# Optimization experiments

Hardware: AMD Instinct MI355X
Metric: run time of the kernel (lower is better)

## Reference

```python
import jax, jax.numpy as jnp
import numpy as np

D_MODEL = 256
N_HEAD = 4
HEAD_DIM = D_MODEL // N_HEAD  # 64


def setup_inputs() -> dict:
    key = jax.random.key(0)
    kx, kw, kb = jax.random.split(key, 3)
    x = jax.random.normal(kx, (4, 2048, D_MODEL), dtype=jnp.float32)
    # nn.Linear(256, 768): weight [768, 256], bias [768]
    bound = 1.0 / np.sqrt(D_MODEL)
    W_qkv = jax.random.uniform(kw, (3 * D_MODEL, D_MODEL), dtype=jnp.float32, minval=-bound, maxval=bound)
    b_qkv = jax.random.uniform(kb, (3 * D_MODEL,), dtype=jnp.float32, minval=-bound, maxval=bound)
    return {"x": x, "W_qkv": W_qkv, "b_qkv": b_qkv}


def reference(x, W_qkv, b_qkv):
    B, S, _ = x.shape
    # fused QKV projection: [B, S, 3*D]
    qkv = jnp.einsum("bsd,ed->bse", x, W_qkv) + b_qkv
    q, k, v = jnp.split(qkv, 3, axis=-1)
    # [B, S, D] -> [B, H, S, Dh]
    def to_heads(t):
        return t.reshape(B, S, N_HEAD, HEAD_DIM).transpose(0, 2, 1, 3)
    q, k, v = to_heads(q), to_heads(k), to_heads(v)
    scale = 1.0 / np.sqrt(HEAD_DIM)
    # scores [B, H, S, S]
    scores = jnp.einsum("bhqd,bhkd->bhqk", q, k) * scale
    attn = jax.nn.softmax(scores, axis=-1)
    out = jnp.einsum("bhqk,bhkd->bhqd", attn, v)  # [B, H, S, Dh]
    return out
```

## Files before the change

### kernel.cpp

```cpp
#include <hip/hip_runtime.h>

#define BB 4
#define SS 2048
#define DM 256
#define NH 4
#define DH 64
#define NROW (BB*SS)
#define NE   (3*DM)
#define BH   (BB*NH)
#define HEAD_ELEMS (BH*SS*DH)
#define NQROWS (BH*SS)

typedef _Float16 half_t;
typedef __attribute__((ext_vector_type(8))) _Float16 half8;
typedef __attribute__((ext_vector_type(4))) _Float16 half4;
typedef __attribute__((ext_vector_type(4))) float floatx4;

#define KPAD 72

__global__ __launch_bounds__(256) void prep(const float* __restrict__ x,
                                            const float* __restrict__ W,
                                            half_t* __restrict__ xh,
                                            half_t* __restrict__ xl,
                                            half_t* __restrict__ wh) {
    int gtid = blockIdx.x * 256 + threadIdx.x;
    {
        int i = gtid * 4;
        float4 v = *(const float4*)&x[i];
        half4 h, l;
        h.x = (half_t)v.x; l.x = (half_t)(v.x - (float)h.x);
        h.y = (half_t)v.y; l.y = (half_t)(v.y - (float)h.y);
        h.z = (half_t)v.z; l.z = (half_t)(v.z - (float)h.z);
        h.w = (half_t)v.w; l.w = (half_t)(v.w - (float)h.w);
        *(half4*)&xh[i] = h;
        *(half4*)&xl[i] = l;
    }
    if (gtid < NE * DM / 4) {
        int i = gtid * 4;
        float4 v = *(const float4*)&W[i];
        half4 h;
        h.x = (half_t)v.x; h.y = (half_t)v.y;
        h.z = (half_t)v.z; h.w = (half_t)v.w;
        *(half4*)&wh[i] = h;
    }
}

__global__ __launch_bounds__(256) void qkv_proj(const half_t* __restrict__ xh,
                                                const half_t* __restrict__ xl,
                                                const half_t* __restrict__ whg,
                                                const float* __restrict__ bias,
                                                half_t* __restrict__ qh,
                                                half_t* __restrict__ kh,
                                                half_t* __restrict__ vt) {
    __shared__ __align__(16) half_t Xh[64 * KPAD];
    __shared__ __align__(16) half_t Xl[64 * KPAD];
    __shared__ __align__(16) half_t Wh[64 * KPAD];

    const int rb   = blockIdx.x * 64;
    const int nb   = blockIdx.y * 64;
    const int tid  = threadIdx.x;
    const int wid  = tid >> 6;
    const int lane = tid & 63;
    const int quad = lane >> 4;
    const int col  = lane & 15;

    floatx4 acc[4];
    #pragma unroll
    for (int t = 0; t < 4; ++t) acc[t] = (floatx4){0.f, 0.f, 0.f, 0.f};

    for (int k0 = 0; k0 < DM; k0 += 64) {
        __syncthreads();
        #pragma unroll
        for (int i = 0; i < 2; ++i) {
            int gi = tid + 256 * i;
            int r  = gi >> 3;
            int c8 = (gi & 7) * 8;
            *(half8*)&Xh[r * KPAD + c8] = *(const half8*)&xh[(size_t)(rb + r) * DM + k0 + c8];
            *(half8*)&Xl[r * KPAD + c8] = *(const half8*)&xl[(size_t)(rb + r) * DM + k0 + c8];
            *(half8*)&Wh[r * KPAD + c8] = *(const half8*)&whg[(size_t)(nb + r) * DM + k0 + c8];
        }
        __syncthreads();

        half8 ah0 = *(const half8*)&Xh[(wid * 16 + col) * KPAD + quad * 8];
        half8 ah1 = *(const half8*)&Xh[(wid * 16 + col) * KPAD + 32 + quad * 8];
        half8 al0 = *(const half8*)&Xl[(wid * 16 + col) * KPAD + quad * 8];
        half8 al1 = *(const half8*)&Xl[(wid * 16 + col) * KPAD + 32 + quad * 8];

        #pragma unroll
        for (int t = 0; t < 4; ++t) {
            half8 bh0 = *(const half8*)&Wh[(t * 16 + col) * KPAD + quad * 8];
            half8 bh1 = *(const half8*)&Wh[(t * 16 + col) * KPAD + 32 + quad * 8];
            acc[t] = __builtin_amdgcn_mfma_f32_16x16x32_f16(ah0, bh0, acc[t], 0, 0, 0);
            acc[t] = __builtin_amdgcn_mfma_f32_16x16x32_f16(ah1, bh1, acc[t], 0, 0, 0);
            acc[t] = __builtin_amdgcn_mfma_f32_16x16x32_f16(al0, bh0, acc[t], 0, 0, 0);
            acc[t] = __builtin_amdgcn_mfma_f32_16x16x32_f16(al1, bh1, acc[t], 0, 0, 0);
        }
    }

    const int part = nb >> 8;
    const int mloc = wid * 16 + quad * 4;
    if (part != 2) {
        #pragma unroll
        for (int t = 0; t < 4; ++t) {
            int e    = nb + t * 16 + col;
            float be = bias[e];
            int dm   = e & 255;
            int h    = dm >> 6;
            int dh   = dm & 63;
            #pragma unroll
            for (int r = 0; r < 4; ++r) {
                int row = rb + mloc + r;
                int b   = row >> 11;
                int s   = row & 2047;
                int bh_ = b * NH + h;
                float val = acc[t][r] + be;
                if (part == 0) {
                    qh[((size_t)bh_ * SS + s) * DH + dh] = (half_t)(val * 0.125f);
                } else {
                    kh[((size_t)bh_ * SS + s) * DH + dh] = (half_t)val;
                }
            }
        }
    } else {
        __syncthreads();
        #pragma unroll
        for (int t = 0; t < 4; ++t) {
            int e    = nb + t * 16 + col;
            float be = bias[e];
            #pragma unroll
            for (int r = 0; r < 4; ++r)
                Xh[(t * 16 + col) * KPAD + mloc + r] = (half_t)(acc[t][r] + be);
        }
        __syncthreads();
        const int b   = rb >> 11;
        const int s0  = rb & 2047;
        const int h   = (nb >> 6) & 3;
        const int bh_ = b * NH + h;
        #pragma unroll
        for (int i = 0; i < 2; ++i) {
            int idx = tid + 256 * i;
            int rr  = idx >> 3;
            int cc8 = (idx & 7) * 8;
            *(half8*)&vt[((size_t)bh_ * DH + rr) * SS + s0 + cc8] =
                *(const half8*)&Xh[rr * KPAD + cc8];
        }
    }
}

__global__ __launch_bounds__(128) void attn(const half_t* __restrict__ qh,
                                            const half_t* __restrict__ kh,
                                            const half_t* __restrict__ vt,
                                            half_t* __restrict__ pO,
                                            float* __restrict__ mst,
                                            float* __restrict__ lst) {
    __shared__ __align__(16) half_t Ks[64 * KPAD];
    __shared__ __align__(16) half_t Vts[64 * KPAD];

    const int q0   = blockIdx.x * 64;
    const int bh   = blockIdx.y;
    const int kz   = blockIdx.z;
    const size_t base = (size_t)bh * SS * DH;
    const int tid  = threadIdx.x;
    const int wid  = tid >> 6;
    const int lane = tid & 63;
    const int quad = lane >> 4;
    const int col  = lane & 15;
    const int ktBeg = kz * (SS / 2);
    const int ktEnd = ktBeg + (SS / 2);

    int srr[4], scc[4];
    #pragma unroll
    for (int i = 0; i < 4; ++i) {
        int gi = tid + 128 * i;
        srr[i] = gi >> 3;
        scc[i] = (gi & 7) * 8;
    }

    half8 bq[2][2];
    #pragma unroll
    for (int st = 0; st < 2; ++st) {
        int s = q0 + wid * 32 + st * 16 + col;
        bq[st][0] = *(const half8*)&qh[base + (size_t)s * DH + quad * 8];
        bq[st][1] = *(const half8*)&qh[base + (size_t)s * DH + 32 + quad * 8];
    }

    half8 ck[4], cv[4], nk[4], nv[4];
    #pragma unroll
    for (int i = 0; i < 4; ++i) {
        ck[i] = *(const half8*)&kh[base + (size_t)(ktBeg + srr[i]) * DH + scc[i]];
        cv[i] = *(const half8*)&vt[base + (size_t)srr[i] * SS + ktBeg + scc[i]];
        nk[i] = ck[i];
        nv[i] = cv[i];
    }

    float m_i[2] = {-3.0e38f, -3.0e38f};
    float l_i[2] = {0.f, 0.f};
    floatx4 o[2][4];
    #pragma unroll
    for (int st = 0; st < 2; ++st)
        #pragma unroll
        for (int dt = 0; dt < 4; ++dt) o[st][dt] = (floatx4){0.f, 0.f, 0.f, 0.f};

    for (int kt = ktBeg; kt < ktEnd; kt += 64) {
        __syncthreads();
        #pragma unroll
        for (int i = 0; i < 4; ++i) {
            *(half8*)&Ks[srr[i] * KPAD + scc[i]]  = ck[i];
            *(half8*)&Vts[srr[i] * KPAD + scc[i]] = cv[i];
        }
        __syncthreads();

        const int ktn = kt + 64;
        if (ktn < ktEnd) {
            #pragma unroll
            for (int i = 0; i < 4; ++i) {
                nk[i] = *(const half8*)&kh[base + (size_t)(ktn + srr[i]) * DH + scc[i]];
                nv[i] = *(const half8*)&vt[base + (size_t)srr[i] * SS + ktn + scc[i]];
            }
        }

        floatx4 sc[2][4];
        #pragma unroll
        for (int t = 0; t < 4; ++t) {
            half8 ak0 = *(const half8*)&Ks[(t * 16 + col) * KPAD + quad * 8];
            half8 ak1 = *(const half8*)&Ks[(t * 16 + col) * KPAD + 32 + quad * 8];
            #pragma unroll
            for (int st = 0; st < 2; ++st) {
                floatx4 c = (floatx4){0.f, 0.f, 0.f, 0.f};
                c = __builtin_amdgcn_mfma_f32_16x16x32_f16(ak0, bq[st][0], c, 0, 0, 0);
                c = __builtin_amdgcn_mfma_f32_16x16x32_f16(ak1, bq[st][1], c, 0, 0, 0);
                sc[st][t] = c;
            }
        }

        half4 pa[2][4];
        #pragma unroll
        for (int st = 0; st < 2; ++st) {
            float mloc = -3.0e38f;
            #pragma unroll
            for (int t = 0; t < 4; ++t)
                #pragma unroll
                for (int r = 0; r < 4; ++r)
                    mloc = fmaxf(mloc, sc[st][t][r]);
            mloc = fmaxf(mloc, __shfl_xor(mloc, 16));
            mloc = fmaxf(mloc, __shfl_xor(mloc, 32));
            float m_new = fmaxf(m_i[st], mloc);
            float alpha = __expf(m_i[st] - m_new);
            m_i[st] = m_new;

            float rsum = 0.f;
            #pragma unroll
            for (int t = 0; t < 4; ++t) {
                float p0 = __expf(sc[st][t][0] - m_new);
                float p1 = __expf(sc[st][t][1] - m_new);
                float p2 = __expf(sc[st][t][2] - m_new);
                float p3 = __expf(sc[st][t][3] - m_new);
                rsum += p0 + p1 + p2 + p3;
                pa[st][t] = (half4){(half_t)p0, (half_t)p1, (half_t)p2, (half_t)p3};
            }
            rsum += __shfl_xor(rsum, 16);
            rsum += __shfl_xor(rsum, 32);
            l_i[st] = l_i[st] * alpha + rsum;

            float ar[4];
            #pragma unroll
            for (int i = 0; i < 4; ++i) ar[i] = __shfl(alpha, quad * 4 + i);
            #pragma unroll
            for (int dt = 0; dt < 4; ++dt)
                #pragma unroll
                for (int i = 0; i < 4; ++i)
                    o[st][dt][i] *= ar[i];
        }

        #pragma unroll
        for (int t = 0; t < 4; ++t) {
            #pragma unroll
            for (int dt = 0; dt < 4; ++dt) {
                half4 bv = *(const half4*)&Vts[(dt * 16 + col) * KPAD + t * 16 + quad * 4];
                #pragma unroll
                for (int st = 0; st < 2; ++st)
                    o[st][dt] = __builtin_amdgcn_mfma_f32_16x16x16f16(pa[st][t], bv, o[st][dt], 0, 0, 0);
            }
        }

        #pragma unroll
        for (int i = 0; i < 4; ++i) { ck[i] = nk[i]; cv[i] = nv[i]; }
    }

    const size_t pbase = (size_t)kz * HEAD_ELEMS + base;
    #pragma unroll
    for (int st = 0; st < 2; ++st) {
        float inv = 1.0f / l_i[st];
        float ir[4];
        #pragma unroll
        for (int i = 0; i < 4; ++i) ir[i] = __shfl(inv, quad * 4 + i);
        #pragma unroll
        for (int dt = 0; dt < 4; ++dt)
            #pragma unroll
            for (int i = 0; i < 4; ++i) {
                int row = q0 + wid * 32 + st * 16 + quad * 4 + i;
                pO[pbase + (size_t)row * DH + dt * 16 + col] = (half_t)(o[st][dt][i] * ir[i]);
            }
        if (quad == 0) {
            int row = q0 + wid * 32 + st * 16 + col;
            int idx = kz * NQROWS + bh * SS + row;
            mst[idx] = m_i[st];
            lst[idx] = l_i[st];
        }
    }
}

__global__ __launch_bounds__(256) void merge(const half_t* __restrict__ pO,
                                             const float* __restrict__ mst,
                                             const float* __restrict__ lst,
                                             float* __restrict__ out) {
    int gid = blockIdx.x * 256 + threadIdx.x;
    int row = gid >> 3;
    int dc  = (gid & 7) * 8;
    float m1 = mst[row], m2 = mst[NQROWS + row];
    float l1 = lst[row], l2 = lst[NQROWS + row];
    float M  = fmaxf(m1, m2);
    float w1 = l1 * __expf(m1 - M);
    float w2 = l2 * __expf(m2 - M);
    float inv = 1.0f / (w1 + w2);
    float a = w1 * inv, b = w2 * inv;
    half8 o1 = *(const half8*)&pO[(size_t)row * DH + dc];
    half8 o2 = *(const half8*)&pO[(size_t)HEAD_ELEMS + (size_t)row * DH + dc];
    float4 r0, r1;
    r0.x = a * (float)o1[0] + b * (float)o2[0];
    r0.y = a * (float)o1[1] + b * (float)o2[1];
    r0.z = a * (float)o1[2] + b * (float)o2[2];
    r0.w = a * (float)o1[3] + b * (float)o2[3];
    r1.x = a * (float)o1[4] + b * (float)o2[4];
    r1.y = a * (float)o1[5] + b * (float)o2[5];
    r1.z = a * (float)o1[6] + b * (float)o2[6];
    r1.w = a * (float)o1[7] + b * (float)o2[7];
    *(float4*)&out[(size_t)row * DH + dc]     = r0;
    *(float4*)&out[(size_t)row * DH + dc + 4] = r1;
}

extern "C" void kernel_launch(void* const* d_in, const int* in_sizes, int n_in,
                              void* d_out, int out_size, void* d_ws, size_t ws_size,
                              hipStream_t stream) {
    const float* x  = (const float*)d_in[0];
    const float* Wq = (const float*)d_in[1];
    const float* bq = (const float*)d_in[2];
    float* out = (float*)d_out;

    half_t* qh  = (half_t*)d_ws;
    half_t* kh  = qh + (size_t)HEAD_ELEMS;
    half_t* vt  = kh + (size_t)HEAD_ELEMS;
    half_t* xh  = vt + (size_t)HEAD_ELEMS;
    half_t* xl  = xh + (size_t)HEAD_ELEMS;
    half_t* whp = xl + (size_t)HEAD_ELEMS;
    half_t* pO  = xh;
    float*  mst = (float*)((char*)d_ws + 21364736);
    float*  lst = mst + 2 * NQROWS;

    prep<<<2048, 256, 0, stream>>>(x, Wq, xh, xl, whp);
    qkv_proj<<<dim3(NROW / 64, NE / 64), 256, 0, stream>>>(xh, xl, whp, bq, qh, kh, vt);
    attn<<<dim3(SS / 64, BH, 2), 128, 0, stream>>>(qh, kh, vt, pO, mst, lst);
    merge<<<1024, 256, 0, stream>>>(pO, mst, lst, out);
}
```

Baseline: 120.6 us.

## Drop LDS staging in projection and attention; load MFMA fragments from global directly

The QKV projection now has each wave load its MFMA operands straight from global memory. Each block covers 128 rows instead of 64, and shared memory is used only for the V transpose. The attention kernel likewise drops its shared-memory K/V tiles and barriers, reading K and V fragments into registers with K prefetched one tile ahead. It also skips the softmax rescale when no row max grows. Together these remove LDS traffic and __syncthreads stalls, at the cost of more uncoalesced global and cache loads and higher register pressure.

```diff
diff --git a/kernel.cpp b/kernel.cpp
--- a/kernel.cpp
+++ b/kernel.cpp
@@ -16,7 +16,7 @@
 typedef __attribute__((ext_vector_type(4))) _Float16 half4;
 typedef __attribute__((ext_vector_type(4))) float floatx4;
 
-#define KPAD 72
+#define VPAD 136
 
 __global__ __launch_bounds__(256) void prep(const float* __restrict__ x,
                                             const float* __restrict__ W,
@@ -52,110 +52,102 @@
                                                 half_t* __restrict__ qh,
                                                 half_t* __restrict__ kh,
                                                 half_t* __restrict__ vt) {
-    __shared__ __align__(16) half_t Xh[64 * KPAD];
-    __shared__ __align__(16) half_t Xl[64 * KPAD];
-    __shared__ __align__(16) half_t Wh[64 * KPAD];
-
-    const int rb   = blockIdx.x * 64;
+    __shared__ __align__(16) half_t Vtile[64 * VPAD];
+
     const int nb   = blockIdx.y * 64;
     const int tid  = threadIdx.x;
     const int wid  = tid >> 6;
     const int lane = tid & 63;
     const int quad = lane >> 4;
     const int col  = lane & 15;
-
-    floatx4 acc[4];
-    #pragma unroll
-    for (int t = 0; t < 4; ++t) acc[t] = (floatx4){0.f, 0.f, 0.f, 0.f};
-
-    for (int k0 = 0; k0 < DM; k0 += 64) {
+    const int rb   = blockIdx.x * 128 + wid * 32;
+
+    floatx4 acc[2][4];
+    #pragma unroll
+    for (int st = 0; st < 2; ++st)
+        #pragma unroll
+        for (int t = 0; t < 4; ++t) acc[st][t] = (floatx4){0.f, 0.f, 0.f, 0.f};
+
+    #pragma unroll
+    for (int k0 = 0; k0 < DM; k0 += 32) {
+        half8 ah[2], al[2], bw[4];
+        #pragma unroll
+        for (int st = 0; st < 2; ++st) {
+            const size_t ro = (size_t)(rb + st * 16 + col) * DM + k0 + quad * 8;
+            ah[st] = *(const half8*)&xh[ro];
+            al[st] = *(const half8*)&xl[ro];
+        }
+        #pragma unroll
+        for (int t = 0; t < 4; ++t)
+            bw[t] = *(const half8*)&whg[(size_t)(nb + t * 16 + col) * DM + k0 + quad * 8];
+        #pragma unroll
+        for (int t = 0; t < 4; ++t)
+            #pragma unroll
+            for (int st = 0; st < 2; ++st) {
+                acc[st][t] = __builtin_amdgcn_mfma_f32_16x16x32_f16(ah[st], bw[t], acc[st][t], 0, 0, 0);
+                acc[st][t] = __builtin_amdgcn_mfma_f32_16x16x32_f16(al[st], bw[t], acc[st][t], 0, 0, 0);
+            }
+    }
+
+    const int part = nb >> 8;
+    if (part != 2) {
+        #pragma unroll
+        for (int st = 0; st < 2; ++st)
+            #pragma unroll
+            for (int t = 0; t < 4; ++t) {
+                int e    = nb + t * 16 + col;
+                float be = bias[e];
+                int dm   = e & 255;
+                int h    = dm >> 6;
+                int dh   = dm & 63;
+                #pragma unroll
+                for (int r = 0; r < 4; ++r) {
+                    int row = rb + st * 16 + quad * 4 + r;
+                    int b   = row >> 11;
+                    int s   = row & 2047;
+                    int bh_ = b * NH + h;
+                    float val = acc[st][t][r] + be;
+                    if (part == 0) {
+                        qh[((size_t)bh_ * SS + s) * DH + dh] = (half_t)(val * 0.125f);
+                    } else {
+                        kh[((size_t)bh_ * SS + s) * DH + dh] = (half_t)val;
+                    }
+                }
+            }
+    } else {
+        #pragma unroll
+        for (int st = 0; st < 2; ++st)
+            #pragma unroll
+            for (int t = 0; t < 4; ++t) {
+                int e    = nb + t * 16 + col;
+                float be = bias[e];
+                #pragma unroll
+                for (int r = 0; r < 4; ++r)
+                    Vtile[(t * 16 + col) * VPAD + wid * 32 + st * 16 + quad * 4 + r] =
+                        (half_t)(acc[st][t][r] + be);
+            }
         __syncthreads();
-        #pragma unroll
-        for (int i = 0; i < 2; ++i) {
-            int gi = tid + 256 * i;
-            int r  = gi >> 3;
-            int c8 = (gi & 7) * 8;
-            *(half8*)&Xh[r * KPAD + c8] = *(const half8*)&xh[(size_t)(rb + r) * DM + k0 + c8];
-            *(half8*)&Xl[r * KPAD + c8] = *(const half8*)&xl[(size_t)(rb + r) * DM + k0 + c8];
-            *(half8*)&Wh[r * KPAD + c8] = *(const half8*)&whg[(size_t)(nb + r) * DM + k0 + c8];
-        }
-        __syncthreads();
-
-        half8 ah0 = *(const half8*)&Xh[(wid * 16 + col) * KPAD + quad * 8];
-        half8 ah1 = *(const half8*)&Xh[(wid * 16 + col) * KPAD + 32 + quad * 8];
-        half8 al0 = *(const half8*)&Xl[(wid * 16 + col) * KPAD + quad * 8];
-        half8 al1 = *(const half8*)&Xl[(wid * 16 + col) * KPAD + 32 + quad * 8];
-
-        #pragma unroll
-        for (int t = 0; t < 4; ++t) {
-            half8 bh0 = *(const half8*)&Wh[(t * 16 + col) * KPAD + quad * 8];
-            half8 bh1 = *(const half8*)&Wh[(t * 16 + col) * KPAD + 32 + quad * 8];
-            acc[t] = __builtin_amdgcn_mfma_f32_16x16x32_f16(ah0, bh0, acc[t], 0, 0, 0);
-            acc[t] = __builtin_amdgcn_mfma_f32_16x16x32_f16(ah1, bh1, acc[t], 0, 0, 0);
-            acc[t] = __builtin_amdgcn_mfma_f32_16x16x32_f16(al0, bh0, acc[t], 0, 0, 0);
-            acc[t] = __builtin_amdgcn_mfma_f32_16x16x32_f16(al1, bh1, acc[t], 0, 0, 0);
-        }
-    }
-
-    const int part = nb >> 8;
-    const int mloc = wid * 16 + quad * 4;
-    if (part != 2) {
-        #pragma unroll
-        for (int t = 0; t < 4; ++t) {
-            int e    = nb + t * 16 + col;
-            float be = bias[e];
-            int dm   = e & 255;
-            int h    = dm >> 6;
-            int dh   = dm & 63;
-            #pragma unroll
-            for (int r = 0; r < 4; ++r) {
-                int row = rb + mloc + r;
-                int b   = row >> 11;
-                int s   = row & 2047;
-                int bh_ = b * NH + h;
-                float val = acc[t][r] + be;
-                if (part == 0) {
-                    qh[((size_t)bh_ * SS + s) * DH + dh] = (half_t)(val * 0.125f);
-                } else {
-                    kh[((size_t)bh_ * SS + s) * DH + dh] = (half_t)val;
-                }
-            }
-        }
-    } else {
-        __syncthreads();
-        #pragma unroll
-        for (int t = 0; t < 4; ++t) {
-            int e    = nb + t * 16 + col;
-            float be = bias[e];
-            #pragma unroll
-            for (int r = 0; r < 4; ++r)
-                Xh[(t * 16 + col) * KPAD + mloc + r] = (half_t)(acc[t][r] + be);
-        }
-        __syncthreads();
-        const int b   = rb >> 11;
-        const int s0  = rb & 2047;
+        const int s0  = (blockIdx.x * 128) & 2047;
+        const int b   = (blockIdx.x * 128) >> 11;
         const int h   = (nb >> 6) & 3;
         const int bh_ = b * NH + h;
         #pragma unroll
-        for (int i = 0; i < 2; ++i) {
-            int idx = tid + 256 * i;
-            int rr  = idx >> 3;
-            int cc8 = (idx & 7) * 8;
-            *(half8*)&vt[((size_t)bh_ * DH + rr) * SS + s0 + cc8] =
-                *(const half8*)&Xh[rr * KPAD + cc8];
-        }
-    }
-}
-
-__global__ __launch_bounds__(128) void attn(const half_t* __restrict__ qh,
-                                            const half_t* __restrict__ kh,
-                                            const half_t* __restrict__ vt,
-                                            half_t* __restrict__ pO,
-                                            float* __restrict__ mst,
-                                            float* __restrict__ lst) {
-    __shared__ __align__(16) half_t Ks[64 * KPAD];
-    __shared__ __align__(16) half_t Vts[64 * KPAD];
-
+        for (int i = 0; i < 4; ++i) {
+            int gi = tid + 256 * i;
+            int rr = gi >> 4;
+            int cc = (gi & 15) * 8;
+            *(half8*)&vt[((size_t)bh_ * DH + rr) * SS + s0 + cc] =
+                *(const half8*)&Vtile[rr * VPAD + cc];
+        }
+    }
+}
+
+__global__ __launch_bounds__(128, 2) void attn(const half_t* __restrict__ qh,
+                                               const half_t* __restrict__ kh,
+                                               const half_t* __restrict__ vt,
+                                               half_t* __restrict__ pO,
+                                               float* __restrict__ mst,
+                                               float* __restrict__ lst) {
     const int q0   = blockIdx.x * 64;
     const int bh   = blockIdx.y;
     const int kz   = blockIdx.z;
@@ -168,14 +160,6 @@
     const int ktBeg = kz * (SS / 2);
     const int ktEnd = ktBeg + (SS / 2);
 
-    int srr[4], scc[4];
-    #pragma unroll
-    for (int i = 0; i < 4; ++i) {
-        int gi = tid + 128 * i;
-        srr[i] = gi >> 3;
-        scc[i] = (gi & 7) * 8;
-    }
-
     half8 bq[2][2];
     #pragma unroll
     for (int st = 0; st < 2; ++st) {
@@ -184,13 +168,12 @@
         bq[st][1] = *(const half8*)&qh[base + (size_t)s * DH + 32 + quad * 8];
     }
 
-    half8 ck[4], cv[4], nk[4], nv[4];
-    #pragma unroll
-    for (int i = 0; i < 4; ++i) {
-        ck[i] = *(const half8*)&kh[base + (size_t)(ktBeg + srr[i]) * DH + scc[i]];
-        cv[i] = *(const half8*)&vt[base + (size_t)srr[i] * SS + ktBeg + scc[i]];
-        nk[i] = ck[i];
-        nv[i] = cv[i];
+    half8 ck[2][4];
+    #pragma unroll
+    for (int t = 0; t < 4; ++t) {
+        const size_t kro = base + (size_t)(ktBeg + t * 16 + col) * DH + quad * 8;
+        ck[0][t] = *(const half8*)&kh[kro];
+        ck[1][t] = *(const half8*)&kh[kro + 32];
     }
 
     float m_i[2] = {-3.0e38f, -3.0e38f};
@@ -202,35 +185,32 @@
         for (int dt = 0; dt < 4; ++dt) o[st][dt] = (floatx4){0.f, 0.f, 0.f, 0.f};
 
     for (int kt = ktBeg; kt < ktEnd; kt += 64) {
-        __syncthreads();
-        #pragma unroll
-        for (int i = 0; i < 4; ++i) {
-            *(half8*)&Ks[srr[i] * KPAD + scc[i]]  = ck[i];
-            *(half8*)&Vts[srr[i] * KPAD + scc[i]] = cv[i];
-        }
-        __syncthreads();
-
-        const int ktn = kt + 64;
-        if (ktn < ktEnd) {
-            #pragma unroll
-            for (int i = 0; i < 4; ++i) {
-                nk[i] = *(const half8*)&kh[base + (size_t)(ktn + srr[i]) * DH + scc[i]];
-                nv[i] = *(const half8*)&vt[base + (size_t)srr[i] * SS + ktn + scc[i]];
-            }
-        }
+        half4 cv[4][4];
+        #pragma unroll
+        for (int t = 0; t < 4; ++t)
+            #pragma unroll
+            for (int dt = 0; dt < 4; ++dt)
+                cv[t][dt] = *(const half4*)&vt[base + (size_t)(dt * 16 + col) * SS +
+                                               kt + t * 16 + quad * 4];
 
         floatx4 sc[2][4];
         #pragma unroll
-        for (int t = 0; t < 4; ++t) {
-            half8 ak0 = *(const half8*)&Ks[(t * 16 + col) * KPAD + quad * 8];
-            half8 ak1 = *(const half8*)&Ks[(t * 16 + col) * KPAD + 32 + quad * 8];
+        for (int t = 0; t < 4; ++t)
             #pragma unroll
             for (int st = 0; st < 2; ++st) {
                 floatx4 c = (floatx4){0.f, 0.f, 0.f, 0.f};
-                c = __builtin_amdgcn_mfma_f32_16x16x32_f16(ak0, bq[st][0], c, 0, 0, 0);
-                c = __builtin_amdgcn_mfma_f32_16x16x32_f16(ak1, bq[st][1], c, 0, 0, 0);
+                c = __builtin_amdgcn_mfma_f32_16x16x32_f16(ck[0][t], bq[st][0], c, 0, 0, 0);
+                c = __builtin_amdgcn_mfma_f32_16x16x32_f16(ck[1][t], bq[st][1], c, 0, 0, 0);
                 sc[st][t] = c;
             }
+
+        const int ktn = (kt + 64 < ktEnd) ? kt + 64 : ktBeg;
+        half8 nk[2][4];
+        #pragma unroll
+        for (int t = 0; t < 4; ++t) {
+            const size_t kro = base + (size_t)(ktn + t * 16 + col) * DH + quad * 8;
+            nk[0][t] = *(const half8*)&kh[kro];
+            nk[1][t] = *(const half8*)&kh[kro + 32];
         }
 
         half4 pa[2][4];
@@ -244,10 +224,23 @@
                     mloc = fmaxf(mloc, sc[st][t][r]);
             mloc = fmaxf(mloc, __shfl_xor(mloc, 16));
             mloc = fmaxf(mloc, __shfl_xor(mloc, 32));
-            float m_new = fmaxf(m_i[st], mloc);
-            float alpha = __expf(m_i[st] - m_new);
-            m_i[st] = m_new;
-
+
+            if (__any(mloc > m_i[st])) {
+                float m_new = fmaxf(m_i[st], mloc);
+                float alpha = __expf(m_i[st] - m_new);
+                m_i[st] = m_new;
+                l_i[st] *= alpha;
+                float ar[4];
+                #pragma unroll
+                for (int i = 0; i < 4; ++i) ar[i] = __shfl(alpha, quad * 4 + i);
+                #pragma unroll
+                for (int dt = 0; dt < 4; ++dt)
+                    #pragma unroll
+                    for (int i = 0; i < 4; ++i)
+                        o[st][dt][i] *= ar[i];
+            }
+
+            float m_new = m_i[st];
             float rsum = 0.f;
             #pragma unroll
             for (int t = 0; t < 4; ++t) {
@@ -260,31 +253,21 @@
             }
             rsum += __shfl_xor(rsum, 16);
             rsum += __shfl_xor(rsum, 32);
-            l_i[st] = l_i[st] * alpha + rsum;
-
-            float ar[4];
-            #pragma unroll
-            for (int i = 0; i < 4; ++i) ar[i] = __shfl(alpha, quad * 4 + i);
-            #pragma unroll
-            for (int dt = 0; dt < 4; ++dt)
-                #pragma unroll
-                for (int i = 0; i < 4; ++i)
-                    o[st][dt][i] *= ar[i];
-        }
-
-        #pragma unroll
-        for (int t = 0; t < 4; ++t) {
+            l_i[st] += rsum;
+        }
+
+        #pragma unroll
+        for (int t = 0; t < 4; ++t)
             #pragma unroll
             for (int dt = 0; dt < 4; ++dt) {
-                half4 bv = *(const half4*)&Vts[(dt * 16 + col) * KPAD + t * 16 + quad * 4];
+                half4 bv = cv[t][dt];
                 #pragma unroll
                 for (int st = 0; st < 2; ++st)
                     o[st][dt] = __builtin_amdgcn_mfma_f32_16x16x16f16(pa[st][t], bv, o[st][dt], 0, 0, 0);
             }
-        }
-
-        #pragma unroll
-        for (int i = 0; i < 4; ++i) { ck[i] = nk[i]; cv[i] = nv[i]; }
+
+        #pragma unroll
+        for (int t = 0; t < 4; ++t) { ck[0][t] = nk[0][t]; ck[1][t] = nk[1][t]; }
     }
 
     const size_t pbase = (size_t)kz * HEAD_ELEMS + base;
@@ -358,7 +341,7 @@
     float*  lst = mst + 2 * NQROWS;
 
     prep<<<2048, 256, 0, stream>>>(x, Wq, xh, xl, whp);
-    qkv_proj<<<dim3(NROW / 64, NE / 64), 256, 0, stream>>>(xh, xl, whp, bq, qh, kh, vt);
+    qkv_proj<<<dim3(NROW / 128, NE / 64), 256, 0, stream>>>(xh, xl, whp, bq, qh, kh, vt);
     attn<<<dim3(SS / 64, BH, 2), 128, 0, stream>>>(qh, kh, vt, pO, mst, lst);
     merge<<<1024, 256, 0, stream>>>(pO, mst, lst, out);
 }
```

New measurement: 183.4 us. 1.52x slower.

## Split attention into up to four KV chunks and restructure QKV projection loads

Applied to the files above, without the earlier changes.

The QKV projection now stages the full 64x256 X tile (high and low halves) in LDS once and reads W fragments straight from global memory, removing the per-k-step barriers. The softmax switches to exp2 with log2(e) folded into the Q scale. The attention kernel drops the separate prefetch registers and gains an occupancy hint. When the workspace is large enough it splits the KV range four ways instead of two, with a generalized merge. The aim is more parallelism and less barrier and register overhead, at the cost of extra partial-output traffic and a merge that now runs runtime-length loops.

```diff
diff --git a/kernel.cpp b/kernel.cpp
--- a/kernel.cpp
+++ b/kernel.cpp
@@ -17,6 +17,8 @@
 typedef __attribute__((ext_vector_type(4))) float floatx4;
 
 #define KPAD 72
+#define XPAD 264
+#define QSCALE 0.1803368801111120f
 
 __global__ __launch_bounds__(256) void prep(const float* __restrict__ x,
                                             const float* __restrict__ W,
@@ -52,9 +54,8 @@
                                                 half_t* __restrict__ qh,
                                                 half_t* __restrict__ kh,
                                                 half_t* __restrict__ vt) {
-    __shared__ __align__(16) half_t Xh[64 * KPAD];
-    __shared__ __align__(16) half_t Xl[64 * KPAD];
-    __shared__ __align__(16) half_t Wh[64 * KPAD];
+    __shared__ __align__(16) half_t Xh2[64 * XPAD];
+    __shared__ __align__(16) half_t Xl2[64 * XPAD];
 
     const int rb   = blockIdx.x * 64;
     const int nb   = blockIdx.y * 64;
@@ -64,36 +65,33 @@
     const int quad = lane >> 4;
     const int col  = lane & 15;
 
+    #pragma unroll
+    for (int i = 0; i < 8; ++i) {
+        int gi = tid + 256 * i;
+        int r  = gi >> 5;
+        int c8 = (gi & 31) * 8;
+        *(half8*)&Xh2[r * XPAD + c8] = *(const half8*)&xh[(size_t)(rb + r) * DM + c8];
+        *(half8*)&Xl2[r * XPAD + c8] = *(const half8*)&xl[(size_t)(rb + r) * DM + c8];
+    }
+    __syncthreads();
+
     floatx4 acc[4];
     #pragma unroll
     for (int t = 0; t < 4; ++t) acc[t] = (floatx4){0.f, 0.f, 0.f, 0.f};
 
-    for (int k0 = 0; k0 < DM; k0 += 64) {
-        __syncthreads();
-        #pragma unroll
-        for (int i = 0; i < 2; ++i) {
-            int gi = tid + 256 * i;
-            int r  = gi >> 3;
-            int c8 = (gi & 7) * 8;
-            *(half8*)&Xh[r * KPAD + c8] = *(const half8*)&xh[(size_t)(rb + r) * DM + k0 + c8];
-            *(half8*)&Xl[r * KPAD + c8] = *(const half8*)&xl[(size_t)(rb + r) * DM + k0 + c8];
-            *(half8*)&Wh[r * KPAD + c8] = *(const half8*)&whg[(size_t)(nb + r) * DM + k0 + c8];
-        }
-        __syncthreads();
-
-        half8 ah0 = *(const half8*)&Xh[(wid * 16 + col) * KPAD + quad * 8];
-        half8 ah1 = *(const half8*)&Xh[(wid * 16 + col) * KPAD + 32 + quad * 8];
-        half8 al0 = *(const half8*)&Xl[(wid * 16 + col) * KPAD + quad * 8];
-        half8 al1 = *(const half8*)&Xl[(wid * 16 + col) * KPAD + 32 + quad * 8];
-
-        #pragma unroll
-        for (int t = 0; t < 4; ++t) {
-            half8 bh0 = *(const half8*)&Wh[(t * 16 + col) * KPAD + quad * 8];
-            half8 bh1 = *(const half8*)&Wh[(t * 16 + col) * KPAD + 32 + quad * 8];
-            acc[t] = __builtin_amdgcn_mfma_f32_16x16x32_f16(ah0, bh0, acc[t], 0, 0, 0);
-            acc[t] = __builtin_amdgcn_mfma_f32_16x16x32_f16(ah1, bh1, acc[t], 0, 0, 0);
-            acc[t] = __builtin_amdgcn_mfma_f32_16x16x32_f16(al0, bh0, acc[t], 0, 0, 0);
-            acc[t] = __builtin_amdgcn_mfma_f32_16x16x32_f16(al1, bh1, acc[t], 0, 0, 0);
+    const int arow = (wid * 16 + col) * XPAD + quad * 8;
+    #pragma unroll
+    for (int k0 = 0; k0 < DM; k0 += 32) {
+        half8 bw[4];
+        #pragma unroll
+        for (int t = 0; t < 4; ++t)
+            bw[t] = *(const half8*)&whg[(size_t)(nb + t * 16 + col) * DM + k0 + quad * 8];
+        half8 ah = *(const half8*)&Xh2[arow + k0];
+        half8 al = *(const half8*)&Xl2[arow + k0];
+        #pragma unroll
+        for (int t = 0; t < 4; ++t) {
+            acc[t] = __builtin_amdgcn_mfma_f32_16x16x32_f16(ah, bw[t], acc[t], 0, 0, 0);
+            acc[t] = __builtin_amdgcn_mfma_f32_16x16x32_f16(al, bw[t], acc[t], 0, 0, 0);
         }
     }
 
@@ -115,7 +113,7 @@
                 int bh_ = b * NH + h;
                 float val = acc[t][r] + be;
                 if (part == 0) {
-                    qh[((size_t)bh_ * SS + s) * DH + dh] = (half_t)(val * 0.125f);
+                    qh[((size_t)bh_ * SS + s) * DH + dh] = (half_t)(val * QSCALE);
                 } else {
                     kh[((size_t)bh_ * SS + s) * DH + dh] = (half_t)val;
                 }
@@ -129,7 +127,7 @@
             float be = bias[e];
             #pragma unroll
             for (int r = 0; r < 4; ++r)
-                Xh[(t * 16 + col) * KPAD + mloc + r] = (half_t)(acc[t][r] + be);
+                Xh2[(t * 16 + col) * KPAD + mloc + r] = (half_t)(acc[t][r] + be);
         }
         __syncthreads();
         const int b   = rb >> 11;
@@ -142,17 +140,17 @@
             int rr  = idx >> 3;
             int cc8 = (idx & 7) * 8;
             *(half8*)&vt[((size_t)bh_ * DH + rr) * SS + s0 + cc8] =
-                *(const half8*)&Xh[rr * KPAD + cc8];
-        }
-    }
-}
-
-__global__ __launch_bounds__(128) void attn(const half_t* __restrict__ qh,
-                                            const half_t* __restrict__ kh,
-                                            const half_t* __restrict__ vt,
-                                            half_t* __restrict__ pO,
-                                            float* __restrict__ mst,
-                                            float* __restrict__ lst) {
+                *(const half8*)&Xh2[rr * KPAD + cc8];
+        }
+    }
+}
+
+__global__ __launch_bounds__(128, 4) void attn(const half_t* __restrict__ qh,
+                                               const half_t* __restrict__ kh,
+                                               const half_t* __restrict__ vt,
+                                               half_t* __restrict__ pO,
+                                               float* __restrict__ mst,
+                                               float* __restrict__ lst) {
     __shared__ __align__(16) half_t Ks[64 * KPAD];
     __shared__ __align__(16) half_t Vts[64 * KPAD];
 
@@ -165,8 +163,9 @@
     const int lane = tid & 63;
     const int quad = lane >> 4;
     const int col  = lane & 15;
-    const int ktBeg = kz * (SS / 2);
-    const int ktEnd = ktBeg + (SS / 2);
+    const int span  = SS / gridDim.z;
+    const int ktBeg = kz * span;
+    const int ktEnd = ktBeg + span;
 
     int srr[4], scc[4];
     #pragma unroll
@@ -184,13 +183,11 @@
         bq[st][1] = *(const half8*)&qh[base + (size_t)s * DH + 32 + quad * 8];
     }
 
-    half8 ck[4], cv[4], nk[4], nv[4];
+    half8 ck[4], cv[4];
     #pragma unroll
     for (int i = 0; i < 4; ++i) {
         ck[i] = *(const half8*)&kh[base + (size_t)(ktBeg + srr[i]) * DH + scc[i]];
         cv[i] = *(const half8*)&vt[base + (size_t)srr[i] * SS + ktBeg + scc[i]];
-        nk[i] = ck[i];
-        nv[i] = cv[i];
     }
 
     float m_i[2] = {-3.0e38f, -3.0e38f};
@@ -214,8 +211,8 @@
         if (ktn < ktEnd) {
             #pragma unroll
             for (int i = 0; i < 4; ++i) {
-                nk[i] = *(const half8*)&kh[base + (size_t)(ktn + srr[i]) * DH + scc[i]];
-                nv[i] = *(const half8*)&vt[base + (size_t)srr[i] * SS + ktn + scc[i]];
+                ck[i] = *(const half8*)&kh[base + (size_t)(ktn + srr[i]) * DH + scc[i]];
+                cv[i] = *(const half8*)&vt[base + (size_t)srr[i] * SS + ktn + scc[i]];
             }
         }
 
@@ -245,16 +242,16 @@
             mloc = fmaxf(mloc, __shfl_xor(mloc, 16));
             mloc = fmaxf(mloc, __shfl_xor(mloc, 32));
             float m_new = fmaxf(m_i[st], mloc);
-            float alpha = __expf(m_i[st] - m_new);
+            float alpha = exp2f(m_i[st] - m_new);
             m_i[st] = m_new;
 
             float rsum = 0.f;
             #pragma unroll
             for (int t = 0; t < 4; ++t) {
-                float p0 = __expf(sc[st][t][0] - m_new);
-                float p1 = __expf(sc[st][t][1] - m_new);
-                float p2 = __expf(sc[st][t][2] - m_new);
-                float p3 = __expf(sc[st][t][3] - m_new);
+                float p0 = exp2f(sc[st][t][0] - m_new);
+                float p1 = exp2f(sc[st][t][1] - m_new);
+                float p2 = exp2f(sc[st][t][2] - m_new);
+                float p3 = exp2f(sc[st][t][3] - m_new);
                 rsum += p0 + p1 + p2 + p3;
                 pa[st][t] = (half4){(half_t)p0, (half_t)p1, (half_t)p2, (half_t)p3};
             }
@@ -282,9 +279,6 @@
                     o[st][dt] = __builtin_amdgcn_mfma_f32_16x16x16f16(pa[st][t], bv, o[st][dt], 0, 0, 0);
             }
         }
-
-        #pragma unroll
-        for (int i = 0; i < 4; ++i) { ck[i] = nk[i]; cv[i] = nv[i]; }
     }
 
     const size_t pbase = (size_t)kz * HEAD_ELEMS + base;
@@ -313,28 +307,30 @@
 __global__ __launch_bounds__(256) void merge(const half_t* __restrict__ pO,
                                              const float* __restrict__ mst,
                                              const float* __restrict__ lst,
-                                             float* __restrict__ out) {
+                                             float* __restrict__ out,
+                                             int nsplit) {
     int gid = blockIdx.x * 256 + threadIdx.x;
     int row = gid >> 3;
     int dc  = (gid & 7) * 8;
-    float m1 = mst[row], m2 = mst[NQROWS + row];
-    float l1 = lst[row], l2 = lst[NQROWS + row];
-    float M  = fmaxf(m1, m2);
-    float w1 = l1 * __expf(m1 - M);
-    float w2 = l2 * __expf(m2 - M);
-    float inv = 1.0f / (w1 + w2);
-    float a = w1 * inv, b = w2 * inv;
-    half8 o1 = *(const half8*)&pO[(size_t)row * DH + dc];
-    half8 o2 = *(const half8*)&pO[(size_t)HEAD_ELEMS + (size_t)row * DH + dc];
+    float M = -3.0e38f;
+    for (int j = 0; j < nsplit; ++j) M = fmaxf(M, mst[j * NQROWS + row]);
+    float w[4];
+    float wsum = 0.f;
+    for (int j = 0; j < nsplit; ++j) {
+        w[j] = lst[j * NQROWS + row] * exp2f(mst[j * NQROWS + row] - M);
+        wsum += w[j];
+    }
+    float inv = 1.0f / wsum;
+    float acc[8] = {0.f, 0.f, 0.f, 0.f, 0.f, 0.f, 0.f, 0.f};
+    for (int j = 0; j < nsplit; ++j) {
+        half8 oj = *(const half8*)&pO[(size_t)j * HEAD_ELEMS + (size_t)row * DH + dc];
+        float wj = w[j];
+        #pragma unroll
+        for (int e = 0; e < 8; ++e) acc[e] += wj * (float)oj[e];
+    }
     float4 r0, r1;
-    r0.x = a * (float)o1[0] + b * (float)o2[0];
-    r0.y = a * (float)o1[1] + b * (float)o2[1];
-    r0.z = a * (float)o1[2] + b * (float)o2[2];
-    r0.w = a * (float)o1[3] + b * (float)o2[3];
-    r1.x = a * (float)o1[4] + b * (float)o2[4];
-    r1.y = a * (float)o1[5] + b * (float)o2[5];
-    r1.z = a * (float)o1[6] + b * (float)o2[6];
-    r1.w = a * (float)o1[7] + b * (float)o2[7];
+    r0.x = acc[0] * inv; r0.y = acc[1] * inv; r0.z = acc[2] * inv; r0.w = acc[3] * inv;
+    r1.x = acc[4] * inv; r1.y = acc[5] * inv; r1.z = acc[6] * inv; r1.w = acc[7] * inv;
     *(float4*)&out[(size_t)row * DH + dc]     = r0;
     *(float4*)&out[(size_t)row * DH + dc + 4] = r1;
 }
@@ -354,11 +350,13 @@
     half_t* xl  = xh + (size_t)HEAD_ELEMS;
     half_t* whp = xl + (size_t)HEAD_ELEMS;
     half_t* pO  = xh;
-    float*  mst = (float*)((char*)d_ws + 21364736);
-    float*  lst = mst + 2 * NQROWS;
+
+    const int nsplit = (ws_size >= 31000000u) ? 4 : 2;
+    float* mst = (float*)((char*)d_ws + 12582912 + (size_t)nsplit * HEAD_ELEMS * 2);
+    float* lst = mst + (size_t)nsplit * NQROWS;
 
     prep<<<2048, 256, 0, stream>>>(x, Wq, xh, xl, whp);
     qkv_proj<<<dim3(NROW / 64, NE / 64), 256, 0, stream>>>(xh, xl, whp, bq, qh, kh, vt);
-    attn<<<dim3(SS / 64, BH, 2), 128, 0, stream>>>(qh, kh, vt, pO, mst, lst);
-    merge<<<1024, 256, 0, stream>>>(pO, mst, lst, out);
-}
+    attn<<<dim3(SS / 64, BH, nsplit), 128, 0, stream>>>(qh, kh, vt, pO, mst, lst);
+    merge<<<1024, 256, 0, stream>>>(pO, mst, lst, out, nsplit);
+}
```

After: 268.6 us. 123% more time.
